# Kernel tuning notes

Hardware: AMD Instinct MI355X
Metric: run time of the kernel (lower is better)

## Reference

```python
import jax, jax.numpy as jnp
import numpy as np

N_NODES = 100_000
N_EDGES = 1_600_000
D_IN = 128
D_HID = 128
LN_EPS = 1e-5


def setup_inputs() -> dict:
    key = jax.random.key(0)
    k1, k2, k3 = jax.random.split(key, 3)
    x = jax.random.normal(k1, (N_NODES, D_IN), dtype=jnp.float32)
    edge_index = jax.random.randint(k2, (2, N_EDGES), 0, N_NODES, dtype=jnp.int32)
    # GCNConv linear weight (glorot-ish) and bias
    W = jax.random.normal(k3, (D_IN, D_HID), dtype=jnp.float32) * (1.0 / np.sqrt(D_IN))
    b = jnp.zeros((D_HID,), dtype=jnp.float32)
    # LayerNorm params
    gamma = jnp.ones((D_HID,), dtype=jnp.float32)
    beta = jnp.zeros((D_HID,), dtype=jnp.float32)
    return {"x": x, "edge_index": edge_index, "W": W, "b": b, "gamma": gamma, "beta": beta}


def reference(x, edge_index, W, b, gamma, beta):
    n = x.shape[0]
    # --- GCNConv: add self-loops, symmetric normalization ---
    loop = jnp.arange(n, dtype=edge_index.dtype)
    row = jnp.concatenate([edge_index[0], loop])  # source j
    col = jnp.concatenate([edge_index[1], loop])  # target i
    deg = jax.ops.segment_sum(jnp.ones(row.shape, x.dtype), col, num_segments=n)
    dinv = jnp.where(deg > 0, jax.lax.rsqrt(deg), jnp.zeros_like(deg))
    norm = dinv[row] * dinv[col]  # [E+N]
    # transform first (input->hidden), then gather-scale-scatter
    h = x @ W  # [N, D_HID]
    msg = h[row] * norm[:, None]  # gather + per-edge scale
    out = jax.ops.segment_sum(msg, col, num_segments=n) + b  # scatter-add
    # --- LayerNorm ---
    mu = jnp.mean(out, axis=-1, keepdims=True)
    var = jnp.mean(jnp.square(out - mu), axis=-1, keepdims=True)
    ln = (out - mu) * jax.lax.rsqrt(var + LN_EPS) * gamma + beta
    # Dropout is identity at inference; ReLU
    return jax.nn.relu(ln)
```

## Files before the change

### kernel.cpp

```cpp
#include <hip/hip_runtime.h>
#include <hip/hip_bf16.h>
#include <math.h>

#define LN_EPS 1e-5f
#define CAP 8192
#define CAPSH 13

typedef __attribute__((ext_vector_type(8))) short short8;
typedef __attribute__((ext_vector_type(4))) float floatx4;

__global__ __launch_bounds__(256) void k_partition(const int* __restrict__ ei, int* __restrict__ bucketCnt,
                                                   unsigned* __restrict__ pk, int E, int chunk,
                                                   const float* __restrict__ W, __hip_bfloat16* __restrict__ Wt) {
    if (blockIdx.x == gridDim.x - 1) {
        for (int i = threadIdx.x; i < 16384; i += 256) {
            int n = i >> 7, k = i & 127;
            Wt[i] = __float2bfloat16(W[k * 128 + n]);
        }
        return;
    }
    __shared__ int ecol[3328];
    __shared__ int esrc[3328];
    __shared__ int h[512];
    __shared__ int base[512];
    int t = threadIdx.x;
    for (int i = t; i < 512; i += 256) h[i] = 0;
    int e0 = blockIdx.x * chunk;
    int e1 = min(e0 + chunk, E);
    int n = e1 - e0;
    __syncthreads();
    for (int i = t; i < n; i += 256) {
        int col = ei[E + e0 + i];
        ecol[i] = col;
        esrc[i] = ei[e0 + i];
        atomicAdd(&h[col >> 8], 1);
    }
    __syncthreads();
    for (int i = t; i < 512; i += 256) {
        if (h[i] > 0) {
            base[i] = atomicAdd(&bucketCnt[i], h[i]);
            h[i] = 0;
        }
    }
    __syncthreads();
    for (int i = t; i < n; i += 256) {
        int col = ecol[i];
        int b = col >> 8;
        int r = base[b] + atomicAdd(&h[b], 1);
        if (r < CAP)
            pk[((unsigned)b << CAPSH) + r] = ((unsigned)(col & 255) << 20) | (unsigned)esrc[i];
    }
}

__global__ __launch_bounds__(256) void k_csr(const unsigned* __restrict__ pk, const int* __restrict__ bucketCnt,
                                             int* __restrict__ cnt, int* __restrict__ rowptr,
                                             float* __restrict__ dinv, int* __restrict__ srcidx, int N) {
    __shared__ int lcnt[256];
    __shared__ int lofs[256];
    __shared__ int s[256];
    int b = blockIdx.x;
    int t = threadIdx.x;
    int ofs = b << CAPSH;
    int cntb = min(bucketCnt[b], CAP);
    lcnt[t] = 0;
    __syncthreads();
    for (int e = t; e < cntb; e += 256)
        atomicAdd(&lcnt[pk[ofs + e] >> 20], 1);
    __syncthreads();
    int v = lcnt[t];
    int pv = (v + 7) & ~7;
    s[t] = pv;
    __syncthreads();
    int val = pv;
    for (int off = 1; off < 256; off <<= 1) {
        int add = (t >= off) ? s[t - off] : 0;
        __syncthreads();
        val += add;
        s[t] = val;
        __syncthreads();
    }
    lofs[t] = val - pv;
    int node = (b << 8) + t;
    if (node < N) {
        cnt[node] = pv;
        rowptr[node] = ofs + lofs[t];
        dinv[node] = rsqrtf((float)(v + 1));
        for (int i = v; i < pv; ++i) {
            int slot = lofs[t] + i;
            if (slot < CAP) srcidx[ofs + slot] = N;
        }
    }
    lcnt[t] = 0;
    __syncthreads();
    for (int e = t; e < cntb; e += 256) {
        unsigned pvv = pk[ofs + e];
        int d = pvv >> 20;
        int r = atomicAdd(&lcnt[d], 1);
        int slot = lofs[d] + r;
        if (slot < CAP) srcidx[ofs + slot] = (int)(pvv & 0xFFFFFu);
    }
}

__global__ __launch_bounds__(256) void k_gemm(const float* __restrict__ x, const __hip_bfloat16* __restrict__ Wt,
                                              const float* __restrict__ dinv, __hip_bfloat16* __restrict__ g, int N) {
    __shared__ unsigned short sA[128 * 128];
    __shared__ unsigned short sB[128 * 128];
    int tid = threadIdx.x;
    int row0 = blockIdx.x * 128;
#pragma unroll
    for (int i = 0; i < 8; ++i) {
        int idx = tid + i * 256;
        int row = idx >> 4;
        int gr = idx & 15;
        int arow = min(row0 + row, N - 1);
        float4 xa = *(const float4*)(x + (size_t)arow * 128 + gr * 8);
        float4 xb = *(const float4*)(x + (size_t)arow * 128 + gr * 8 + 4);
        union { short8 s; __hip_bfloat16 h[8]; } a;
        a.h[0] = __float2bfloat16(xa.x); a.h[1] = __float2bfloat16(xa.y);
        a.h[2] = __float2bfloat16(xa.z); a.h[3] = __float2bfloat16(xa.w);
        a.h[4] = __float2bfloat16(xb.x); a.h[5] = __float2bfloat16(xb.y);
        a.h[6] = __float2bfloat16(xb.z); a.h[7] = __float2bfloat16(xb.w);
        int grs = gr ^ (row & 15);
        *(short8*)(&sA[row * 128 + grs * 8]) = a.s;
        *(short8*)(&sB[row * 128 + grs * 8]) = *(const short8*)(Wt + (size_t)row * 128 + gr * 8);
    }
    __syncthreads();
    int lane = tid & 63;
    int wv = tid >> 6;
    int m = lane & 15;
    int q = lane >> 4;
    floatx4 acc[2][8];
#pragma unroll
    for (int mt = 0; mt < 2; ++mt)
#pragma unroll
        for (int nt = 0; nt < 8; ++nt) acc[mt][nt] = (floatx4){0.f, 0.f, 0.f, 0.f};
#pragma unroll
    for (int kc = 0; kc < 4; ++kc) {
        int gg = kc * 4 + q;
        short8 afrag[2], bfrag[8];
#pragma unroll
        for (int mt = 0; mt < 2; ++mt) {
            int row = wv * 32 + mt * 16 + m;
            afrag[mt] = *(const short8*)(&sA[row * 128 + (gg ^ (row & 15)) * 8]);
        }
#pragma unroll
        for (int nt = 0; nt < 8; ++nt) {
            int n = nt * 16 + m;
            bfrag[nt] = *(const short8*)(&sB[n * 128 + (gg ^ (n & 15)) * 8]);
        }
#pragma unroll
        for (int mt = 0; mt < 2; ++mt)
#pragma unroll
            for (int nt = 0; nt < 8; ++nt)
                acc[mt][nt] = __builtin_amdgcn_mfma_f32_16x16x32_bf16(afrag[mt], bfrag[nt], acc[mt][nt], 0, 0, 0);
    }
#pragma unroll
    for (int mt = 0; mt < 2; ++mt) {
#pragma unroll
        for (int i = 0; i < 4; ++i) {
            int row = row0 + wv * 32 + mt * 16 + q * 4 + i;
            if (row < N) {
                float dv = dinv[row];
                __hip_bfloat16* gp = g + (size_t)row * 128;
#pragma unroll
                for (int nt = 0; nt < 8; ++nt)
                    gp[nt * 16 + m] = __float2bfloat16(acc[mt][nt][i] * dv);
            }
        }
    }
}

#define LOAD8(P, OFF) \
    unsigned P##0 = g1[((size_t)(unsigned)__builtin_amdgcn_readlane(myidx, j + OFF + 0)) * 64u + lane]; \
    unsigned P##1 = g1[((size_t)(unsigned)__builtin_amdgcn_readlane(myidx, j + OFF + 1)) * 64u + lane]; \
    unsigned P##2 = g1[((size_t)(unsigned)__builtin_amdgcn_readlane(myidx, j + OFF + 2)) * 64u + lane]; \
    unsigned P##3 = g1[((size_t)(unsigned)__builtin_amdgcn_readlane(myidx, j + OFF + 3)) * 64u + lane]; \
    unsigned P##4 = g1[((size_t)(unsigned)__builtin_amdgcn_readlane(myidx, j + OFF + 4)) * 64u + lane]; \
    unsigned P##5 = g1[((size_t)(unsigned)__builtin_amdgcn_readlane(myidx, j + OFF + 5)) * 64u + lane]; \
    unsigned P##6 = g1[((size_t)(unsigned)__builtin_amdgcn_readlane(myidx, j + OFF + 6)) * 64u + lane]; \
    unsigned P##7 = g1[((size_t)(unsigned)__builtin_amdgcn_readlane(myidx, j + OFF + 7)) * 64u + lane];

#define ACC8(P) \
    ax += ((__uint_as_float(P##0 << 16) + __uint_as_float(P##1 << 16)) + \
           (__uint_as_float(P##2 << 16) + __uint_as_float(P##3 << 16))) + \
          ((__uint_as_float(P##4 << 16) + __uint_as_float(P##5 << 16)) + \
           (__uint_as_float(P##6 << 16) + __uint_as_float(P##7 << 16))); \
    ay += ((__uint_as_float(P##0 & 0xFFFF0000u) + __uint_as_float(P##1 & 0xFFFF0000u)) + \
           (__uint_as_float(P##2 & 0xFFFF0000u) + __uint_as_float(P##3 & 0xFFFF0000u))) + \
          ((__uint_as_float(P##4 & 0xFFFF0000u) + __uint_as_float(P##5 & 0xFFFF0000u)) + \
           (__uint_as_float(P##6 & 0xFFFF0000u) + __uint_as_float(P##7 & 0xFFFF0000u)));

__global__ __launch_bounds__(256) void k_agg_ln(const __hip_bfloat16* __restrict__ g, const int* __restrict__ srcidx,
                                                const int* __restrict__ rowptr, const int* __restrict__ cnt,
                                                const float* __restrict__ dinv, const float* __restrict__ bias,
                                                const float* __restrict__ gamma, const float* __restrict__ beta,
                                                float* __restrict__ out, int N) {
    int wid = (int)((blockIdx.x * 256u + threadIdx.x) >> 6);
    int lane = threadIdx.x & 63;
    if (wid >= N) return;
    const unsigned* g1 = (const unsigned*)g;
    unsigned sv = g1[(size_t)wid * 64 + lane];
    float ax = __uint_as_float(sv << 16);
    float ay = __uint_as_float(sv & 0xFFFF0000u);
    int start = __builtin_amdgcn_readfirstlane(rowptr[wid]);
    int pcnt = __builtin_amdgcn_readfirstlane(cnt[wid]);
    int end = start + pcnt;
    for (int eb = start; eb < end; eb += 64) {
        int myidx = srcidx[eb + lane];
        int nb = min(64, end - eb);
        int j = 0;
        for (; j + 16 <= nb; j += 16) {
            LOAD8(pa, 0)
            LOAD8(pb, 8)
            ACC8(pa)
            ACC8(pb)
        }
        for (; j < nb; j += 8) {
            LOAD8(pc, 0)
            ACC8(pc)
        }
    }
    float di = dinv[wid];
    int c0 = lane * 2;
    float vx = ax * di + bias[c0];
    float vy = ay * di + bias[c0 + 1];
    float sum = vx + vy, sq = vx * vx + vy * vy;
#pragma unroll
    for (int off = 32; off > 0; off >>= 1) {
        sum += __shfl_xor(sum, off, 64);
        sq += __shfl_xor(sq, off, 64);
    }
    float mu = sum * (1.0f / 128.0f);
    float var = sq * (1.0f / 128.0f) - mu * mu;
    float rstd = rsqrtf(var + LN_EPS);
    float o0 = fmaxf((vx - mu) * rstd * gamma[c0] + beta[c0], 0.f);
    float o1 = fmaxf((vy - mu) * rstd * gamma[c0 + 1] + beta[c0 + 1], 0.f);
    ((float2*)out)[(size_t)wid * 64 + lane] = make_float2(o0, o1);
}

extern "C" void kernel_launch(void* const* d_in, const int* in_sizes, int n_in,
                              void* d_out, int out_size, void* d_ws, size_t ws_size,
                              hipStream_t stream) {
    const float* x = (const float*)d_in[0];
    const int* ei = (const int*)d_in[1];
    const float* W = (const float*)d_in[2];
    const float* bias = (const float*)d_in[3];
    const float* gamma = (const float*)d_in[4];
    const float* beta = (const float*)d_in[5];
    float* out = (float*)d_out;

    int N = in_sizes[0] / 128;
    int E = in_sizes[1] / 2;
    int NBUCK = (N + 255) / 256;

    char* p = (char*)d_ws;
    auto alloc = [&](size_t bytes) {
        char* r = p;
        p += (bytes + 255) & ~(size_t)255;
        return r;
    };
    int* cnt = (int*)alloc((size_t)N * 4);
    int* rowptr = (int*)alloc((size_t)N * 4);
    float* dinv = (float*)alloc((size_t)N * 4);
    int* bucketCnt = (int*)alloc(512 * 4);
    __hip_bfloat16* Wt = (__hip_bfloat16*)alloc(128 * 128 * 2);
    int* srcidx = (int*)alloc(((size_t)NBUCK * CAP + 64) * 4);
    __hip_bfloat16* gbuf = (__hip_bfloat16*)alloc((size_t)(N + 1) * 128 * 2);
    unsigned* pk = (unsigned*)gbuf;

    const int NBLK = 512;
    int chunk = (E + NBLK - 1) / NBLK;

    hipMemsetAsync(bucketCnt, 0, 512 * 4, stream);
    hipMemsetAsync(gbuf + (size_t)N * 128, 0, 256, stream);
    k_partition<<<NBLK + 1, 256, 0, stream>>>(ei, bucketCnt, pk, E, chunk, W, Wt);
    k_csr<<<NBUCK, 256, 0, stream>>>(pk, bucketCnt, cnt, rowptr, dinv, srcidx, N);
    k_gemm<<<(N + 127) / 128, 256, 0, stream>>>(x, Wt, dinv, gbuf, N);
    k_agg_ln<<<(N + 3) / 4, 256, 0, stream>>>(gbuf, srcidx, rowptr, cnt, dinv, bias, gamma, beta, out, N);
}
```

Measured before the change: 220.2 us.

## Merge CSR build and GEMM into one launch, compute degrees in partition

```diff
diff --git a/kernel.cpp b/kernel.cpp
--- a/kernel.cpp
+++ b/kernel.cpp
@@ -10,7 +10,8 @@
 typedef __attribute__((ext_vector_type(4))) float floatx4;
 
 __global__ __launch_bounds__(256) void k_partition(const int* __restrict__ ei, int* __restrict__ bucketCnt,
-                                                   unsigned* __restrict__ pk, int E, int chunk,
+                                                   unsigned* __restrict__ pk, int* __restrict__ cnt,
+                                                   int E, int chunk,
                                                    const float* __restrict__ W, __hip_bfloat16* __restrict__ Wt) {
     if (blockIdx.x == gridDim.x - 1) {
         for (int i = threadIdx.x; i < 16384; i += 256) {
@@ -19,8 +20,8 @@
         }
         return;
     }
-    __shared__ int ecol[3328];
-    __shared__ int esrc[3328];
+    __shared__ int ecol[1664];
+    __shared__ int esrc[1664];
     __shared__ int h[512];
     __shared__ int base[512];
     int t = threadIdx.x;
@@ -34,6 +35,7 @@
         ecol[i] = col;
         esrc[i] = ei[e0 + i];
         atomicAdd(&h[col >> 8], 1);
+        atomicAdd(&cnt[col], 1);
     }
     __syncthreads();
     for (int i = t; i < 512; i += 256) {
@@ -52,133 +54,140 @@
     }
 }
 
-__global__ __launch_bounds__(256) void k_csr(const unsigned* __restrict__ pk, const int* __restrict__ bucketCnt,
-                                             int* __restrict__ cnt, int* __restrict__ rowptr,
-                                             float* __restrict__ dinv, int* __restrict__ srcidx, int N) {
-    __shared__ int lcnt[256];
-    __shared__ int lofs[256];
-    __shared__ int s[256];
-    int b = blockIdx.x;
-    int t = threadIdx.x;
-    int ofs = b << CAPSH;
-    int cntb = min(bucketCnt[b], CAP);
-    lcnt[t] = 0;
-    __syncthreads();
-    for (int e = t; e < cntb; e += 256)
-        atomicAdd(&lcnt[pk[ofs + e] >> 20], 1);
-    __syncthreads();
-    int v = lcnt[t];
-    int pv = (v + 7) & ~7;
-    s[t] = pv;
-    __syncthreads();
-    int val = pv;
-    for (int off = 1; off < 256; off <<= 1) {
-        int add = (t >= off) ? s[t - off] : 0;
-        __syncthreads();
-        val += add;
-        s[t] = val;
-        __syncthreads();
-    }
-    lofs[t] = val - pv;
-    int node = (b << 8) + t;
-    if (node < N) {
-        cnt[node] = pv;
-        rowptr[node] = ofs + lofs[t];
-        dinv[node] = rsqrtf((float)(v + 1));
-        for (int i = v; i < pv; ++i) {
-            int slot = lofs[t] + i;
-            if (slot < CAP) srcidx[ofs + slot] = N;
-        }
-    }
-    lcnt[t] = 0;
-    __syncthreads();
-    for (int e = t; e < cntb; e += 256) {
-        unsigned pvv = pk[ofs + e];
-        int d = pvv >> 20;
-        int r = atomicAdd(&lcnt[d], 1);
-        int slot = lofs[d] + r;
-        if (slot < CAP) srcidx[ofs + slot] = (int)(pvv & 0xFFFFFu);
-    }
-}
-
-__global__ __launch_bounds__(256) void k_gemm(const float* __restrict__ x, const __hip_bfloat16* __restrict__ Wt,
-                                              const float* __restrict__ dinv, __hip_bfloat16* __restrict__ g, int N) {
-    __shared__ unsigned short sA[128 * 128];
-    __shared__ unsigned short sB[128 * 128];
-    int tid = threadIdx.x;
-    int row0 = blockIdx.x * 128;
-#pragma unroll
-    for (int i = 0; i < 8; ++i) {
-        int idx = tid + i * 256;
-        int row = idx >> 4;
-        int gr = idx & 15;
-        int arow = min(row0 + row, N - 1);
-        float4 xa = *(const float4*)(x + (size_t)arow * 128 + gr * 8);
-        float4 xb = *(const float4*)(x + (size_t)arow * 128 + gr * 8 + 4);
-        union { short8 s; __hip_bfloat16 h[8]; } a;
-        a.h[0] = __float2bfloat16(xa.x); a.h[1] = __float2bfloat16(xa.y);
-        a.h[2] = __float2bfloat16(xa.z); a.h[3] = __float2bfloat16(xa.w);
-        a.h[4] = __float2bfloat16(xb.x); a.h[5] = __float2bfloat16(xb.y);
-        a.h[6] = __float2bfloat16(xb.z); a.h[7] = __float2bfloat16(xb.w);
-        int grs = gr ^ (row & 15);
-        *(short8*)(&sA[row * 128 + grs * 8]) = a.s;
-        *(short8*)(&sB[row * 128 + grs * 8]) = *(const short8*)(Wt + (size_t)row * 128 + gr * 8);
-    }
-    __syncthreads();
-    int lane = tid & 63;
-    int wv = tid >> 6;
-    int m = lane & 15;
-    int q = lane >> 4;
-    floatx4 acc[2][8];
-#pragma unroll
-    for (int mt = 0; mt < 2; ++mt)
-#pragma unroll
-        for (int nt = 0; nt < 8; ++nt) acc[mt][nt] = (floatx4){0.f, 0.f, 0.f, 0.f};
-#pragma unroll
-    for (int kc = 0; kc < 4; ++kc) {
-        int gg = kc * 4 + q;
-        short8 afrag[2], bfrag[8];
+__global__ __launch_bounds__(256) void k_dinv(const int* __restrict__ cnt, float* __restrict__ dinv,
+                                              unsigned* __restrict__ gdummy, int N) {
+    int i = blockIdx.x * 256 + threadIdx.x;
+    if (i < N) dinv[i] = rsqrtf((float)(cnt[i] + 1));
+    if (blockIdx.x == 0 && threadIdx.x < 64) gdummy[threadIdx.x] = 0;
+}
+
+__global__ __launch_bounds__(256) void k_csr_gemm(const unsigned* __restrict__ pk, const int* __restrict__ bucketCnt,
+                                                  int2* __restrict__ rowcnt, int* __restrict__ srcidx,
+                                                  const float* __restrict__ x, const __hip_bfloat16* __restrict__ Wt,
+                                                  const float* __restrict__ dinv, __hip_bfloat16* __restrict__ g,
+                                                  int N, int NB) {
+    __shared__ unsigned short smem[2 * 128 * 128];
+    if ((int)blockIdx.x < NB) {
+        int* lcnt = (int*)smem;
+        int* lofs = lcnt + 256;
+        int* sc = lofs + 256;
+        int b = blockIdx.x;
+        int t = threadIdx.x;
+        int ofs = b << CAPSH;
+        int cntb = min(bucketCnt[b], CAP);
+        lcnt[t] = 0;
+        __syncthreads();
+        for (int e = t; e < cntb; e += 256)
+            atomicAdd(&lcnt[pk[ofs + e] >> 20], 1);
+        __syncthreads();
+        int v = lcnt[t];
+        int pv = (v + 7) & ~7;
+        sc[t] = pv;
+        __syncthreads();
+        int val = pv;
+        for (int off = 1; off < 256; off <<= 1) {
+            int add = (t >= off) ? sc[t - off] : 0;
+            __syncthreads();
+            val += add;
+            sc[t] = val;
+            __syncthreads();
+        }
+        lofs[t] = val - pv;
+        int node = (b << 8) + t;
+        if (node < N) {
+            rowcnt[node] = make_int2(ofs + lofs[t], pv);
+            for (int i = v; i < pv; ++i) {
+                int slot = lofs[t] + i;
+                if (slot < CAP) srcidx[ofs + slot] = N;
+            }
+        }
+        lcnt[t] = 0;
+        __syncthreads();
+        for (int e = t; e < cntb; e += 256) {
+            unsigned pvv = pk[ofs + e];
+            int d = pvv >> 20;
+            int r = atomicAdd(&lcnt[d], 1);
+            int slot = lofs[d] + r;
+            if (slot < CAP) srcidx[ofs + slot] = (int)(pvv & 0xFFFFFu);
+        }
+    } else {
+        unsigned short* sA = smem;
+        unsigned short* sB = smem + 128 * 128;
+        int tid = threadIdx.x;
+        int row0 = ((int)blockIdx.x - NB) * 128;
+#pragma unroll
+        for (int i = 0; i < 8; ++i) {
+            int idx = tid + i * 256;
+            int row = idx >> 4;
+            int gr = idx & 15;
+            int arow = min(row0 + row, N - 1);
+            float4 xa = *(const float4*)(x + (size_t)arow * 128 + gr * 8);
+            float4 xb = *(const float4*)(x + (size_t)arow * 128 + gr * 8 + 4);
+            union { short8 s; __hip_bfloat16 h[8]; } a;
+            a.h[0] = __float2bfloat16(xa.x); a.h[1] = __float2bfloat16(xa.y);
+            a.h[2] = __float2bfloat16(xa.z); a.h[3] = __float2bfloat16(xa.w);
+            a.h[4] = __float2bfloat16(xb.x); a.h[5] = __float2bfloat16(xb.y);
+            a.h[6] = __float2bfloat16(xb.z); a.h[7] = __float2bfloat16(xb.w);
+            int grs = gr ^ (row & 15);
+            *(short8*)(&sA[row * 128 + grs * 8]) = a.s;
+            *(short8*)(&sB[row * 128 + grs * 8]) = *(const short8*)(Wt + (size_t)row * 128 + gr * 8);
+        }
+        __syncthreads();
+        int lane = tid & 63;
+        int wv = tid >> 6;
+        int m = lane & 15;
+        int q = lane >> 4;
+        floatx4 acc[2][8];
+#pragma unroll
+        for (int mt = 0; mt < 2; ++mt)
+#pragma unroll
+            for (int nt = 0; nt < 8; ++nt) acc[mt][nt] = (floatx4){0.f, 0.f, 0.f, 0.f};
+#pragma unroll
+        for (int kc = 0; kc < 4; ++kc) {
+            int gg = kc * 4 + q;
+            short8 afrag[2], bfrag[8];
+#pragma unroll
+            for (int mt = 0; mt < 2; ++mt) {
+                int row = wv * 32 + mt * 16 + m;
+                afrag[mt] = *(const short8*)(&sA[row * 128 + (gg ^ (row & 15)) * 8]);
+            }
+#pragma unroll
+            for (int nt = 0; nt < 8; ++nt) {
+                int n = nt * 16 + m;
+                bfrag[nt] = *(const short8*)(&sB[n * 128 + (gg ^ (n & 15)) * 8]);
+            }
+#pragma unroll
+            for (int mt = 0; mt < 2; ++mt)
+#pragma unroll
+                for (int nt = 0; nt < 8; ++nt)
+                    acc[mt][nt] = __builtin_amdgcn_mfma_f32_16x16x32_bf16(afrag[mt], bfrag[nt], acc[mt][nt], 0, 0, 0);
+        }
 #pragma unroll
         for (int mt = 0; mt < 2; ++mt) {
-            int row = wv * 32 + mt * 16 + m;
-            afrag[mt] = *(const short8*)(&sA[row * 128 + (gg ^ (row & 15)) * 8]);
-        }
-#pragma unroll
-        for (int nt = 0; nt < 8; ++nt) {
-            int n = nt * 16 + m;
-            bfrag[nt] = *(const short8*)(&sB[n * 128 + (gg ^ (n & 15)) * 8]);
-        }
-#pragma unroll
-        for (int mt = 0; mt < 2; ++mt)
-#pragma unroll
-            for (int nt = 0; nt < 8; ++nt)
-                acc[mt][nt] = __builtin_amdgcn_mfma_f32_16x16x32_bf16(afrag[mt], bfrag[nt], acc[mt][nt], 0, 0, 0);
-    }
-#pragma unroll
-    for (int mt = 0; mt < 2; ++mt) {
-#pragma unroll
-        for (int i = 0; i < 4; ++i) {
-            int row = row0 + wv * 32 + mt * 16 + q * 4 + i;
-            if (row < N) {
-                float dv = dinv[row];
-                __hip_bfloat16* gp = g + (size_t)row * 128;
-#pragma unroll
-                for (int nt = 0; nt < 8; ++nt)
-                    gp[nt * 16 + m] = __float2bfloat16(acc[mt][nt][i] * dv);
-            }
-        }
-    }
-}
-
-#define LOAD8(P, OFF) \
-    unsigned P##0 = g1[((size_t)(unsigned)__builtin_amdgcn_readlane(myidx, j + OFF + 0)) * 64u + lane]; \
-    unsigned P##1 = g1[((size_t)(unsigned)__builtin_amdgcn_readlane(myidx, j + OFF + 1)) * 64u + lane]; \
-    unsigned P##2 = g1[((size_t)(unsigned)__builtin_amdgcn_readlane(myidx, j + OFF + 2)) * 64u + lane]; \
-    unsigned P##3 = g1[((size_t)(unsigned)__builtin_amdgcn_readlane(myidx, j + OFF + 3)) * 64u + lane]; \
-    unsigned P##4 = g1[((size_t)(unsigned)__builtin_amdgcn_readlane(myidx, j + OFF + 4)) * 64u + lane]; \
-    unsigned P##5 = g1[((size_t)(unsigned)__builtin_amdgcn_readlane(myidx, j + OFF + 5)) * 64u + lane]; \
-    unsigned P##6 = g1[((size_t)(unsigned)__builtin_amdgcn_readlane(myidx, j + OFF + 6)) * 64u + lane]; \
-    unsigned P##7 = g1[((size_t)(unsigned)__builtin_amdgcn_readlane(myidx, j + OFF + 7)) * 64u + lane];
+#pragma unroll
+            for (int i = 0; i < 4; ++i) {
+                int row = row0 + wv * 32 + mt * 16 + q * 4 + i;
+                if (row < N) {
+                    float dv = dinv[row];
+                    __hip_bfloat16* gp = g + (size_t)row * 128;
+#pragma unroll
+                    for (int nt = 0; nt < 8; ++nt)
+                        gp[nt * 16 + m] = __float2bfloat16(acc[mt][nt][i] * dv);
+                }
+            }
+        }
+    }
+}
+
+#define LOAD8(P, B) \
+    unsigned P##0 = g1[((size_t)(unsigned)__builtin_amdgcn_readlane(myidx, (B) + 0)) * 64u + lane]; \
+    unsigned P##1 = g1[((size_t)(unsigned)__builtin_amdgcn_readlane(myidx, (B) + 1)) * 64u + lane]; \
+    unsigned P##2 = g1[((size_t)(unsigned)__builtin_amdgcn_readlane(myidx, (B) + 2)) * 64u + lane]; \
+    unsigned P##3 = g1[((size_t)(unsigned)__builtin_amdgcn_readlane(myidx, (B) + 3)) * 64u + lane]; \
+    unsigned P##4 = g1[((size_t)(unsigned)__builtin_amdgcn_readlane(myidx, (B) + 4)) * 64u + lane]; \
+    unsigned P##5 = g1[((size_t)(unsigned)__builtin_amdgcn_readlane(myidx, (B) + 5)) * 64u + lane]; \
+    unsigned P##6 = g1[((size_t)(unsigned)__builtin_amdgcn_readlane(myidx, (B) + 6)) * 64u + lane]; \
+    unsigned P##7 = g1[((size_t)(unsigned)__builtin_amdgcn_readlane(myidx, (B) + 7)) * 64u + lane];
 
 #define ACC8(P) \
     ax += ((__uint_as_float(P##0 << 16) + __uint_as_float(P##1 << 16)) + \
@@ -191,7 +200,7 @@
            (__uint_as_float(P##6 & 0xFFFF0000u) + __uint_as_float(P##7 & 0xFFFF0000u)));
 
 __global__ __launch_bounds__(256) void k_agg_ln(const __hip_bfloat16* __restrict__ g, const int* __restrict__ srcidx,
-                                                const int* __restrict__ rowptr, const int* __restrict__ cnt,
+                                                const int2* __restrict__ rowcnt,
                                                 const float* __restrict__ dinv, const float* __restrict__ bias,
                                                 const float* __restrict__ gamma, const float* __restrict__ beta,
                                                 float* __restrict__ out, int N) {
@@ -202,28 +211,40 @@
     unsigned sv = g1[(size_t)wid * 64 + lane];
     float ax = __uint_as_float(sv << 16);
     float ay = __uint_as_float(sv & 0xFFFF0000u);
-    int start = __builtin_amdgcn_readfirstlane(rowptr[wid]);
-    int pcnt = __builtin_amdgcn_readfirstlane(cnt[wid]);
+    int2 rc = rowcnt[wid];
+    int start = __builtin_amdgcn_readfirstlane(rc.x);
+    int pcnt = __builtin_amdgcn_readfirstlane(rc.y);
     int end = start + pcnt;
     for (int eb = start; eb < end; eb += 64) {
         int myidx = srcidx[eb + lane];
         int nb = min(64, end - eb);
-        int j = 0;
-        for (; j + 16 <= nb; j += 16) {
+        if (nb >= 24) {
             LOAD8(pa, 0)
             LOAD8(pb, 8)
+            LOAD8(pc, 16)
             ACC8(pa)
             ACC8(pb)
-        }
-        for (; j < nb; j += 8) {
-            LOAD8(pc, 0)
             ACC8(pc)
+            for (int j = 24; j + 8 <= nb; j += 8) {
+                LOAD8(pd, j)
+                ACC8(pd)
+            }
+        } else if (nb == 16) {
+            LOAD8(pe, 0)
+            LOAD8(pf, 8)
+            ACC8(pe)
+            ACC8(pf)
+        } else {
+            LOAD8(pg, 0)
+            ACC8(pg)
         }
     }
     float di = dinv[wid];
-    int c0 = lane * 2;
-    float vx = ax * di + bias[c0];
-    float vy = ay * di + bias[c0 + 1];
+    float2 bi = ((const float2*)bias)[lane];
+    float2 ga = ((const float2*)gamma)[lane];
+    float2 be = ((const float2*)beta)[lane];
+    float vx = ax * di + bi.x;
+    float vy = ay * di + bi.y;
     float sum = vx + vy, sq = vx * vx + vy * vy;
 #pragma unroll
     for (int off = 32; off > 0; off >>= 1) {
@@ -233,8 +254,8 @@
     float mu = sum * (1.0f / 128.0f);
     float var = sq * (1.0f / 128.0f) - mu * mu;
     float rstd = rsqrtf(var + LN_EPS);
-    float o0 = fmaxf((vx - mu) * rstd * gamma[c0] + beta[c0], 0.f);
-    float o1 = fmaxf((vy - mu) * rstd * gamma[c0 + 1] + beta[c0 + 1], 0.f);
+    float o0 = fmaxf((vx - mu) * rstd * ga.x + be.x, 0.f);
+    float o1 = fmaxf((vy - mu) * rstd * ga.y + be.y, 0.f);
     ((float2*)out)[(size_t)wid * 64 + lane] = make_float2(o0, o1);
 }
 
@@ -260,21 +281,22 @@
         return r;
     };
     int* cnt = (int*)alloc((size_t)N * 4);
-    int* rowptr = (int*)alloc((size_t)N * 4);
+    size_t cntPad = ((size_t)N * 4 + 255) & ~(size_t)255;
+    int* bucketCnt = (int*)alloc(512 * 4);
+    int2* rowcnt = (int2*)alloc((size_t)N * 8);
     float* dinv = (float*)alloc((size_t)N * 4);
-    int* bucketCnt = (int*)alloc(512 * 4);
     __hip_bfloat16* Wt = (__hip_bfloat16*)alloc(128 * 128 * 2);
     int* srcidx = (int*)alloc(((size_t)NBUCK * CAP + 64) * 4);
     __hip_bfloat16* gbuf = (__hip_bfloat16*)alloc((size_t)(N + 1) * 128 * 2);
-    unsigned* pk = (unsigned*)gbuf;
-
-    const int NBLK = 512;
+    unsigned* pk = (unsigned*)d_out;
+
+    const int NBLK = 1024;
     int chunk = (E + NBLK - 1) / NBLK;
-
-    hipMemsetAsync(bucketCnt, 0, 512 * 4, stream);
-    hipMemsetAsync(gbuf + (size_t)N * 128, 0, 256, stream);
-    k_partition<<<NBLK + 1, 256, 0, stream>>>(ei, bucketCnt, pk, E, chunk, W, Wt);
-    k_csr<<<NBUCK, 256, 0, stream>>>(pk, bucketCnt, cnt, rowptr, dinv, srcidx, N);
-    k_gemm<<<(N + 127) / 128, 256, 0, stream>>>(x, Wt, dinv, gbuf, N);
-    k_agg_ln<<<(N + 3) / 4, 256, 0, stream>>>(gbuf, srcidx, rowptr, cnt, dinv, bias, gamma, beta, out, N);
-}
+    int GB = (N + 127) / 128;
+
+    hipMemsetAsync(cnt, 0, cntPad + 512 * 4, stream);
+    k_partition<<<NBLK + 1, 256, 0, stream>>>(ei, bucketCnt, pk, cnt, E, chunk, W, Wt);
+    k_dinv<<<(N + 255) / 256, 256, 0, stream>>>(cnt, dinv, (unsigned*)(gbuf + (size_t)N * 128), N);
+    k_csr_gemm<<<NBUCK + GB, 256, 0, stream>>>(pk, bucketCnt, rowcnt, srcidx, x, Wt, dinv, gbuf, N, NBUCK);
+    k_agg_ln<<<(N + 3) / 4, 256, 0, stream>>>(gbuf, srcidx, rowcnt, dinv, bias, gamma, beta, out, N);
+}
```

After: 281.7 us. 27.9% more time.
